# Kernel tuning notes

Measured on AMD Instinct MI355X. Metric: run time of the kernel, lower is better.

## Reference

```python
import jax, jax.numpy as jnp
import numpy as np

N_NODES = 50000
N_EDGES = 800000
IN_F = 64
OUT_F = 64


def setup_inputs() -> dict:
    key = jax.random.key(0)
    k_x, k_r, k_c, k_v, k_w, k_b = jax.random.split(key, 6)
    x = jax.random.normal(k_x, (N_NODES, IN_F), dtype=jnp.float32)
    edge_row = jax.random.randint(k_r, (N_EDGES,), 0, N_NODES, dtype=jnp.int32)
    edge_col = jax.random.randint(k_c, (N_EDGES,), 0, N_NODES, dtype=jnp.int32)
    edge_val = jax.random.uniform(k_v, (N_EDGES,), dtype=jnp.float32)
    weight = jax.random.normal(k_w, (IN_F, OUT_F), dtype=jnp.float32) * (2.0 / (IN_F + OUT_F)) ** 0.5
    bias = jax.random.normal(k_b, (OUT_F,), dtype=jnp.float32) * 0.1
    return {"x": x, "edge_row": edge_row, "edge_col": edge_col,
            "edge_val": edge_val, "weight": weight, "bias": bias}


def reference(x, edge_row, edge_col, edge_val, weight, bias):
    # support = x @ W  : dense GEMM  [N, out]
    support = jnp.matmul(x, weight)
    # output = spmm(adj, support): for each edge (r, c, v): out[r] += v * support[c]
    gathered = support[edge_col] * edge_val[:, None]  # [E, out]
    output = jax.ops.segment_sum(gathered, edge_row, num_segments=N_NODES)
    return output + bias
```

## Files before the change

### kernel.cpp

```cpp
#include <hip/hip_runtime.h>
#include <hip/hip_bf16.h>

#define N_NODES 50000
#define N_EDGES 800000
#define NF 64
#define BUCK_SHIFT 6
#define BUCK_SIZE 64
#define NBUK ((N_NODES + BUCK_SIZE - 1) / BUCK_SIZE)
#define CAP 1280
#define CHUNK 4096
#define BIN_BLOCKS ((N_EDGES + CHUNK - 1) / CHUNK)
#define GEMM_BLOCKS 828
#define TABW (NBUK + 1)
#define PER ((NBUK + 255) / 256)
#define EPT (CHUNK / 256)

__global__ __launch_bounds__(256) void produce(
    const float* __restrict__ x, const int* __restrict__ erow,
    const int* __restrict__ ecol, const float* __restrict__ eval,
    const float* __restrict__ w, int2* __restrict__ stage1,
    int* __restrict__ tab, __hip_bfloat16* __restrict__ support) {
  __shared__ __align__(16) char smem[CHUNK * 8 + NBUK * 4 + 16];
  const int tid = threadIdx.x;
  const int lane = tid & 63;
  const int wave = tid >> 6;

  if (blockIdx.x < BIN_BLOCKS) {
    int2* sorted = (int2*)smem;
    int* hist = (int*)(smem + CHUNK * 8);
    int* wsum = hist + NBUK;

    for (int t = tid; t < NBUK; t += 256) hist[t] = 0;
    __syncthreads();

    const int e0 = blockIdx.x * CHUNK;
    const int e1 = min(e0 + CHUNK, N_EDGES);

    int rj[EPT], cj[EPT];
    float vj[EPT];
#pragma unroll
    for (int j = 0; j < EPT; ++j) {
      const int e = e0 + tid + j * 256;
      const bool ok = e < e1;
      rj[j] = ok ? erow[e] : -1;
      cj[j] = ok ? ecol[e] : 0;
      vj[j] = ok ? eval[e] : 0.f;
      if (ok) atomicAdd(&hist[rj[j] >> BUCK_SHIFT], 1);
    }
    __syncthreads();

    int loc[PER];
    int tsum = 0;
    const int i0 = tid * PER;
#pragma unroll
    for (int j = 0; j < PER; ++j) {
      const int idx = i0 + j;
      const int v = (idx < NBUK) ? hist[idx] : 0;
      loc[j] = tsum;
      tsum += v;
    }
    int sc = tsum;
#pragma unroll
    for (int off = 1; off < 64; off <<= 1) {
      const int up = __shfl_up(sc, off, 64);
      if (lane >= off) sc += up;
    }
    if (lane == 63) wsum[wave] = sc;
    __syncthreads();
    int woff = 0;
#pragma unroll
    for (int k = 0; k < 4; ++k) woff += (k < wave) ? wsum[k] : 0;
    const int texcl = woff + sc - tsum;

    int* gt = tab + (size_t)blockIdx.x * TABW;
#pragma unroll
    for (int j = 0; j < PER; ++j) {
      const int idx = i0 + j;
      if (idx < NBUK) {
        const int o = texcl + loc[j];
        hist[idx] = o;
        gt[idx] = o;
      }
    }
    if (tid == 0) gt[NBUK] = e1 - e0;
    __syncthreads();

#pragma unroll
    for (int j = 0; j < EPT; ++j) {
      if (rj[j] >= 0) {
        const int b = rj[j] >> BUCK_SHIFT;
        const int p = atomicAdd(&hist[b], 1);
        sorted[p] = make_int2(((rj[j] & (BUCK_SIZE - 1)) << 16) | cj[j],
                              __float_as_int(vj[j]));
      }
    }
    __syncthreads();

    const int n = e1 - e0;
    int2* gs = stage1 + (size_t)blockIdx.x * CHUNK;
    for (int i = tid; i < n; i += 256) gs[i] = sorted[i];
  } else {
    float wcol[NF];
#pragma unroll
    for (int k = 0; k < NF; ++k) wcol[k] = w[k * NF + lane];

    const int wid = (blockIdx.x - BIN_BLOCKS) * 4 + wave;
    const int nw = GEMM_BLOCKS * 4;
    for (int row = wid; row < N_NODES; row += 2 * nw) {
      const int rA = __builtin_amdgcn_readfirstlane(row);
      const int rB_raw = row + nw;
      const bool hasB = rB_raw < N_NODES;
      const int rB = __builtin_amdgcn_readfirstlane(hasB ? rB_raw : rA);
      const float* xA = x + (size_t)rA * NF;
      const float* xB = x + (size_t)rB * NF;
      float a0 = 0.f, a1 = 0.f, a2 = 0.f, a3 = 0.f;
      float b0 = 0.f, b1 = 0.f, b2 = 0.f, b3 = 0.f;
#pragma unroll
      for (int k = 0; k < NF; k += 4) {
        a0 = fmaf(xA[k + 0], wcol[k + 0], a0);
        b0 = fmaf(xB[k + 0], wcol[k + 0], b0);
        a1 = fmaf(xA[k + 1], wcol[k + 1], a1);
        b1 = fmaf(xB[k + 1], wcol[k + 1], b1);
        a2 = fmaf(xA[k + 2], wcol[k + 2], a2);
        b2 = fmaf(xB[k + 2], wcol[k + 2], b2);
        a3 = fmaf(xA[k + 3], wcol[k + 3], a3);
        b3 = fmaf(xB[k + 3], wcol[k + 3], b3);
      }
      support[(size_t)rA * NF + lane] = __float2bfloat16((a0 + a1) + (a2 + a3));
      if (hasB)
        support[(size_t)rB * NF + lane] =
            __float2bfloat16((b0 + b1) + (b2 + b3));
    }
  }
}

__global__ __launch_bounds__(512) void spmm_sorted(
    const __hip_bfloat16* __restrict__ support, const int* __restrict__ tab,
    const int2* __restrict__ stage1, const float* __restrict__ bias,
    float* __restrict__ out) {
  __shared__ int2 srt[CAP];
  __shared__ int segpos[BIN_BLOCKS + 1];
  __shared__ int segst[BIN_BLOCKS];
  __shared__ int rcnt[BUCK_SIZE];
  __shared__ int rofs[BUCK_SIZE];
  __shared__ int rcur[BUCK_SIZE];
  __shared__ int wsum[8];
  const int b = blockIdx.x;
  const int tid = threadIdx.x;
  const int lane = tid & 63;
  const int wave = tid >> 6;

  if (tid < BUCK_SIZE) rcnt[tid] = 0;

  int st = 0, c = 0;
  if (tid < BIN_BLOCKS) {
    const int* gt = tab + (size_t)tid * TABW;
    st = gt[b];
    c = gt[b + 1] - st;
  }
  int sc = c;
#pragma unroll
  for (int off = 1; off < 64; off <<= 1) {
    const int up = __shfl_up(sc, off, 64);
    if (lane >= off) sc += up;
  }
  if (lane == 63) wsum[wave] = sc;
  __syncthreads();
  int woff = 0;
#pragma unroll
  for (int k = 0; k < 8; ++k) woff += (k < wave) ? wsum[k] : 0;
  if (tid < BIN_BLOCKS) {
    segpos[tid] = woff + sc - c;
    segst[tid] = st;
  }
  if (tid == 511) segpos[BIN_BLOCKS] = woff + sc;
  __syncthreads();

  const int cnt = min(segpos[BIN_BLOCKS], CAP);

  int2 mreg[3];
#pragma unroll
  for (int q = 0; q < 3; ++q) {
    const int i = tid + q * 512;
    mreg[q] = make_int2(-1, 0);
    if (i < cnt) {
      int lo = 0, hi = BIN_BLOCKS - 1;
      while (lo < hi) {
        const int mid = (lo + hi + 1) >> 1;
        if (segpos[mid] <= i) lo = mid;
        else hi = mid - 1;
      }
      const int k = i - segpos[lo];
      const int2 m = stage1[(size_t)lo * CHUNK + segst[lo] + k];
      mreg[q] = m;
      atomicAdd(&rcnt[m.x >> 16], 1);
    }
  }
  __syncthreads();

  if (tid < 64) {
    const int v = rcnt[lane];
    int s2 = v;
#pragma unroll
    for (int off = 1; off < 64; off <<= 1) {
      const int up = __shfl_up(s2, off, 64);
      if (lane >= off) s2 += up;
    }
    rofs[lane] = s2 - v;
    rcur[lane] = s2 - v;
  }
  __syncthreads();

#pragma unroll
  for (int q = 0; q < 3; ++q) {
    if (mreg[q].x >= 0) {
      const int p = atomicAdd(&rcur[mreg[q].x >> 16], 1);
      srt[p] = mreg[q];
    }
  }
  __syncthreads();

  const int row0 = b << BUCK_SHIFT;
  const float bv = bias[lane];
#pragma unroll
  for (int rr = 0; rr < 8; ++rr) {
    const int rl = wave * 8 + rr;
    const int row = row0 + rl;
    if (row >= N_NODES) break;
    const int s = __builtin_amdgcn_readfirstlane(rofs[rl]);
    const int e = __builtin_amdgcn_readfirstlane(rofs[rl] + rcnt[rl]);
    float a0 = 0.f, a1 = 0.f, a2 = 0.f, a3 = 0.f;
    int i = s;
    for (; i + 4 <= e; i += 4) {
      const int2 m0 = srt[i + 0];
      const int2 m1 = srt[i + 1];
      const int2 m2 = srt[i + 2];
      const int2 m3 = srt[i + 3];
      const float s0 = __bfloat162float(support[(size_t)(m0.x & 0xFFFF) * NF + lane]);
      const float s1 = __bfloat162float(support[(size_t)(m1.x & 0xFFFF) * NF + lane]);
      const float s2 = __bfloat162float(support[(size_t)(m2.x & 0xFFFF) * NF + lane]);
      const float s3 = __bfloat162float(support[(size_t)(m3.x & 0xFFFF) * NF + lane]);
      a0 = fmaf(__int_as_float(m0.y), s0, a0);
      a1 = fmaf(__int_as_float(m1.y), s1, a1);
      a2 = fmaf(__int_as_float(m2.y), s2, a2);
      a3 = fmaf(__int_as_float(m3.y), s3, a3);
    }
    for (; i < e; ++i) {
      const int2 m0 = srt[i];
      a0 = fmaf(__int_as_float(m0.y),
                __bfloat162float(support[(size_t)(m0.x & 0xFFFF) * NF + lane]),
                a0);
    }
    out[(size_t)row * NF + lane] = ((a0 + a1) + (a2 + a3)) + bv;
  }
}

extern "C" void kernel_launch(void* const* d_in, const int* in_sizes, int n_in,
                              void* d_out, int out_size, void* d_ws,
                              size_t ws_size, hipStream_t stream) {
  const float* x = (const float*)d_in[0];
  const int* erow = (const int*)d_in[1];
  const int* ecol = (const int*)d_in[2];
  const float* eval = (const float*)d_in[3];
  const float* w = (const float*)d_in[4];
  const float* bias = (const float*)d_in[5];
  float* out = (float*)d_out;

  char* ws = (char*)d_ws;
  __hip_bfloat16* support = (__hip_bfloat16*)(ws);
  int2* stage1 = (int2*)(ws + 6400000);
  int* tab = (int*)(ws + 12822528);

  produce<<<BIN_BLOCKS + GEMM_BLOCKS, 256, 0, stream>>>(
      x, erow, ecol, eval, w, stage1, tab, support);
  spmm_sorted<<<NBUK, 512, 0, stream>>>(support, tab, stage1, bias, out);
}
```

Baseline: 118.7 us.

## Gather four edges per wave with 8-byte bf16 loads in SpMM

Reorganizes the SpMM inner loop so each wave splits into four 16-lane groups. Each group processes a different edge and each lane loads four bf16 features as one 8-byte load, where before each lane issued a 2-byte load for one feature. Partial sums are combined with cross-group shuffles, and the result is written as float4. This cuts the number of gather instructions and widens each memory access, at the cost of shuffle reductions and idle lanes when a row has few edges.

```diff
diff --git a/kernel.cpp b/kernel.cpp
--- a/kernel.cpp
+++ b/kernel.cpp
@@ -220,8 +220,10 @@
   }
   __syncthreads();
 
+  const int grp = lane >> 4;
+  const int sub = lane & 15;
   const int row0 = b << BUCK_SHIFT;
-  const float bv = bias[lane];
+  const float4 bv4 = reinterpret_cast<const float4*>(bias)[sub];
 #pragma unroll
   for (int rr = 0; rr < 8; ++rr) {
     const int rl = wave * 8 + rr;
@@ -231,27 +233,48 @@
     const int e = __builtin_amdgcn_readfirstlane(rofs[rl] + rcnt[rl]);
     float a0 = 0.f, a1 = 0.f, a2 = 0.f, a3 = 0.f;
     int i = s;
-    for (; i + 4 <= e; i += 4) {
-      const int2 m0 = srt[i + 0];
-      const int2 m1 = srt[i + 1];
-      const int2 m2 = srt[i + 2];
-      const int2 m3 = srt[i + 3];
-      const float s0 = __bfloat162float(support[(size_t)(m0.x & 0xFFFF) * NF + lane]);
-      const float s1 = __bfloat162float(support[(size_t)(m1.x & 0xFFFF) * NF + lane]);
-      const float s2 = __bfloat162float(support[(size_t)(m2.x & 0xFFFF) * NF + lane]);
-      const float s3 = __bfloat162float(support[(size_t)(m3.x & 0xFFFF) * NF + lane]);
-      a0 = fmaf(__int_as_float(m0.y), s0, a0);
-      a1 = fmaf(__int_as_float(m1.y), s1, a1);
-      a2 = fmaf(__int_as_float(m2.y), s2, a2);
-      a3 = fmaf(__int_as_float(m3.y), s3, a3);
-    }
-    for (; i < e; ++i) {
-      const int2 m0 = srt[i];
-      a0 = fmaf(__int_as_float(m0.y),
-                __bfloat162float(support[(size_t)(m0.x & 0xFFFF) * NF + lane]),
-                a0);
-    }
-    out[(size_t)row * NF + lane] = ((a0 + a1) + (a2 + a3)) + bv;
+    for (; i + 16 <= e; i += 16) {
+#pragma unroll
+      for (int q = 0; q < 4; ++q) {
+        const int2 m = srt[i + 4 * q + grp];
+        const float v = __int_as_float(m.y);
+        const uint2 t = *reinterpret_cast<const uint2*>(
+            support + (size_t)(m.x & 0xFFFF) * NF + sub * 4);
+        a0 = fmaf(v, __int_as_float(t.x << 16), a0);
+        a1 = fmaf(v, __int_as_float((int)(t.x & 0xFFFF0000u)), a1);
+        a2 = fmaf(v, __int_as_float(t.y << 16), a2);
+        a3 = fmaf(v, __int_as_float((int)(t.y & 0xFFFF0000u)), a3);
+      }
+    }
+    for (; i < e; i += 4) {
+      const int idx = i + grp;
+      if (idx < e) {
+        const int2 m = srt[idx];
+        const float v = __int_as_float(m.y);
+        const uint2 t = *reinterpret_cast<const uint2*>(
+            support + (size_t)(m.x & 0xFFFF) * NF + sub * 4);
+        a0 = fmaf(v, __int_as_float(t.x << 16), a0);
+        a1 = fmaf(v, __int_as_float((int)(t.x & 0xFFFF0000u)), a1);
+        a2 = fmaf(v, __int_as_float(t.y << 16), a2);
+        a3 = fmaf(v, __int_as_float((int)(t.y & 0xFFFF0000u)), a3);
+      }
+    }
+    a0 += __shfl_xor(a0, 16, 64);
+    a1 += __shfl_xor(a1, 16, 64);
+    a2 += __shfl_xor(a2, 16, 64);
+    a3 += __shfl_xor(a3, 16, 64);
+    a0 += __shfl_xor(a0, 32, 64);
+    a1 += __shfl_xor(a1, 32, 64);
+    a2 += __shfl_xor(a2, 32, 64);
+    a3 += __shfl_xor(a3, 32, 64);
+    if (grp == 0) {
+      float4 o;
+      o.x = a0 + bv4.x;
+      o.y = a1 + bv4.y;
+      o.z = a2 + bv4.z;
+      o.w = a3 + bv4.w;
+      reinterpret_cast<float4*>(out + (size_t)row * NF)[sub] = o;
+    }
   }
 }
 
```

Measured after the change: 111.2 us, median of 2. 1.07x faster.
